# Performance work log

Measured on AMD Instinct MI355X. Metric: run time of the kernel, lower is better.

The kernel has to match this reference:

```python
import jax, jax.numpy as jnp
import numpy as np

EMBED_DIM = 512

def setup_inputs() -> dict:
    key = jax.random.key(0)
    ks = jax.random.split(key, 8)
    B, N, M, C = 4, 4096, 4096, EMBED_DIM
    s = 1.0 / np.sqrt(C)
    return {
        "rgb_features": jax.random.normal(ks[0], (B, N, C), jnp.float32),
        "depth_features": jax.random.normal(ks[1], (B, M, C), jnp.float32),
        "Wq": jax.random.normal(ks[2], (C, C), jnp.float32) * s,
        "bq": jnp.zeros((C,), jnp.float32),
        "Wk": jax.random.normal(ks[3], (C, C), jnp.float32) * s,
        "bk": jnp.zeros((C,), jnp.float32),
        "Wv": jax.random.normal(ks[4], (C, C), jnp.float32) * s,
        "bv": jnp.zeros((C,), jnp.float32),
    }

def reference(rgb_features, depth_features, Wq, bq, Wk, bk, Wv, bv):
    C = rgb_features.shape[-1]
    scale = C ** (-0.5)
    Q = rgb_features @ Wq + bq          # [B, N, C]
    K = depth_features @ Wk + bk        # [B, M, C]
    V = depth_features @ Wv + bv        # [B, M, C]
    scores = jnp.einsum('bnc,bmc->bnm', Q, K) * scale
    attn = jax.nn.softmax(scores, axis=-1)
    return jnp.einsum('bnm,bmc->bnc', attn, V)
```

## Files before the change

kernel.cpp:

```cpp
#include <hip/hip_runtime.h>
#include <hip/hip_bf16.h>
#include <stdint.h>


typedef unsigned short u16;
typedef __attribute__((ext_vector_type(8))) short bf16x8;
typedef __attribute__((ext_vector_type(16))) float f32x16;
typedef __attribute__((ext_vector_type(4))) unsigned short u16x4;

#define GLD_LDS16(g, l)                                                        \
  __builtin_amdgcn_global_load_lds(                                            \
      (const __attribute__((address_space(1))) unsigned int*)(g),              \
      (__attribute__((address_space(3))) unsigned int*)(l), 16, 0, 0)

__device__ __forceinline__ u16 f2bf(float f) {
  unsigned x = __float_as_uint(f);
  return (u16)((x + 0x7fffu + ((x >> 16) & 1u)) >> 16);
}
__device__ __forceinline__ float bf2f(short s) {
  return __uint_as_float((unsigned)(unsigned short)s << 16);
}

template <int TM, int TN, int BIAS_MODE, int OUT_MODE, int MINW>
__global__ __launch_bounds__(256, MINW) void gemm32(
    const u16* __restrict__ A, const u16* __restrict__ Bm,
    const float* __restrict__ bias, void* __restrict__ Cv, int M, int N, int K,
    long long sAb, long long sBb, long long sCb, float scale) {
  constexpr int WROWS = TM / 2;
  constexpr int WCOLS = TN / 2;
  constexpr int MSUB = WROWS / 32;
  constexpr int NSUB = WCOLS / 32;
  constexpr int CA = TM / 64;
  constexpr int CB = TN / 64;

  const int bz = blockIdx.z;
  A += (size_t)bz * sAb;
  Bm += (size_t)bz * sBb;

  const int bm = blockIdx.y * TM;
  const int bn = blockIdx.x * TN;

  __shared__ u16 As[2][TM * 32];
  __shared__ u16 Bs[2][TN * 32];

  const int tid = threadIdx.x;
  const int wave = tid >> 6;
  const int lane = tid & 63;
  const int ln31 = lane & 31;
  const int half = lane >> 5;
  const int wr = wave >> 1;
  const int wc = wave & 1;

  const int rowA = lane >> 2;
  const int swz = ((lane & 3) ^ ((rowA + (rowA >> 2)) & 3)) * 8;
  const int gl = (ln31 + (ln31 >> 2)) & 3;

  f32x16 acc[MSUB][NSUB] = {};

  auto stage = [&](int buf, int k0) {
#pragma unroll
    for (int r = 0; r < CA; ++r) {
      const int ch = wave * CA + r;
      GLD_LDS16(A + (size_t)(bm + ch * 16 + rowA) * K + k0 + swz,
                As[buf] + ch * 16 * 32);
    }
#pragma unroll
    for (int r = 0; r < CB; ++r) {
      const int ch = wave * CB + r;
      GLD_LDS16(Bm + (size_t)(bn + ch * 16 + rowA) * K + k0 + swz,
                Bs[buf] + ch * 16 * 32);
    }
  };

  const int niter = K >> 5;
  stage(0, 0);
  for (int it = 0; it < niter; ++it) {
    __syncthreads();
    if (it + 1 < niter) stage((it + 1) & 1, (it + 1) * 32);
    const int buf = it & 1;
#pragma unroll
    for (int kc = 0; kc < 2; ++kc) {
      const int p = ((kc * 2 + half) ^ gl) * 8;
      bf16x8 af[MSUB], bfv[NSUB];
#pragma unroll
      for (int mt = 0; mt < MSUB; ++mt)
        af[mt] =
            *(const bf16x8*)&As[buf][(wr * WROWS + mt * 32 + ln31) * 32 + p];
#pragma unroll
      for (int nt = 0; nt < NSUB; ++nt)
        bfv[nt] =
            *(const bf16x8*)&Bs[buf][(wc * WCOLS + nt * 32 + ln31) * 32 + p];
#pragma unroll
      for (int mt = 0; mt < MSUB; ++mt)
#pragma unroll
        for (int nt = 0; nt < NSUB; ++nt)
          acc[mt][nt] = __builtin_amdgcn_mfma_f32_32x32x16_bf16(
              af[mt], bfv[nt], acc[mt][nt], 0, 0, 0);
    }
  }

  const int crow0 = bm + wr * WROWS + 4 * half;
  const int ccol0 = bn + wc * WCOLS + ln31;
#pragma unroll
  for (int mt = 0; mt < MSUB; ++mt) {
#pragma unroll
    for (int nt = 0; nt < NSUB; ++nt) {
      const int col = ccol0 + nt * 32;
#pragma unroll
      for (int r = 0; r < 16; ++r) {
        const int row = crow0 + mt * 32 + (r & 3) + 8 * (r >> 2);
        float v = acc[mt][nt][r];
        if constexpr (BIAS_MODE == 1) v += bias[col];
        if constexpr (BIAS_MODE == 2) v += bias[row];
        const size_t idx = (size_t)bz * (size_t)sCb + (size_t)row * N + col;
        if constexpr (OUT_MODE == 0)
          ((u16*)Cv)[idx] = f2bf(v);
        else if constexpr (OUT_MODE == 1)
          ((float*)Cv)[idx] = v;
        else
          ((u16*)Cv)[idx] = f2bf(__expf(v * scale));
      }
    }
  }
}

__global__ __launch_bounds__(256, 2) void pv_gemm(
    const u16* __restrict__ P, const u16* __restrict__ Vt,
    float* __restrict__ O) {
  const int bz = blockIdx.z;
  const u16* A = P + (size_t)bz * (4096ull * 4096ull);
  const u16* B = Vt + (size_t)bz * (512ull * 4096ull);
  float* Ob = O + (size_t)bz * (4096ull * 512ull);

  const int bm = blockIdx.y * 64;
  const int bn = blockIdx.x * 256;

  __shared__ u16 As[2][64 * 32];
  __shared__ u16 Bs[2][256 * 32];
  __shared__ float den_s[64];

  const int tid = threadIdx.x;
  const int wave = tid >> 6;
  const int lane = tid & 63;
  const int ln31 = lane & 31;
  const int half = lane >> 5;

  const int rowA = lane >> 2;
  const int swz = ((lane & 3) ^ ((rowA + (rowA >> 2)) & 3)) * 8;
  const int gl = (ln31 + (ln31 >> 2)) & 3;

  f32x16 acc[2][2] = {};
  float rsum[2] = {0.f, 0.f};

  auto stage = [&](int buf, int k0) {
    GLD_LDS16(A + (size_t)(bm + wave * 16 + rowA) * 4096 + k0 + swz,
              As[buf] + wave * 16 * 32);
#pragma unroll
    for (int r = 0; r < 4; ++r) {
      const int ch = wave * 4 + r;
      GLD_LDS16(B + (size_t)(bn + ch * 16 + rowA) * 4096 + k0 + swz,
                Bs[buf] + ch * 16 * 32);
    }
  };

  stage(0, 0);
  for (int it = 0; it < 128; ++it) {
    __syncthreads();
    if (it + 1 < 128) stage((it + 1) & 1, (it + 1) * 32);
    const int buf = it & 1;
#pragma unroll
    for (int kc = 0; kc < 2; ++kc) {
      const int p = ((kc * 2 + half) ^ gl) * 8;
      bf16x8 af[2], bfv[2];
#pragma unroll
      for (int mt = 0; mt < 2; ++mt)
        af[mt] = *(const bf16x8*)&As[buf][(mt * 32 + ln31) * 32 + p];
#pragma unroll
      for (int nt = 0; nt < 2; ++nt)
        bfv[nt] =
            *(const bf16x8*)&Bs[buf][(wave * 64 + nt * 32 + ln31) * 32 + p];
#pragma unroll
      for (int mt = 0; mt < 2; ++mt) {
#pragma unroll
        for (int j = 0; j < 8; ++j) rsum[mt] += bf2f(af[mt][j]);
#pragma unroll
        for (int nt = 0; nt < 2; ++nt)
          acc[mt][nt] = __builtin_amdgcn_mfma_f32_32x32x16_bf16(
              af[mt], bfv[nt], acc[mt][nt], 0, 0, 0);
      }
    }
  }

#pragma unroll
  for (int mt = 0; mt < 2; ++mt) rsum[mt] += __shfl_xor(rsum[mt], 32, 64);
  __syncthreads();
  if (wave == 0 && half == 0) {
    den_s[ln31] = rsum[0];
    den_s[32 + ln31] = rsum[1];
  }
  __syncthreads();

  const int crow0 = 4 * half;
  const int ccol0 = bn + wave * 64 + ln31;
#pragma unroll
  for (int mt = 0; mt < 2; ++mt) {
#pragma unroll
    for (int r = 0; r < 16; ++r) {
      const int rl = crow0 + mt * 32 + (r & 3) + 8 * (r >> 2);
      const float rd = 1.0f / den_s[rl];
#pragma unroll
      for (int nt = 0; nt < 2; ++nt)
        Ob[(size_t)(bm + rl) * 512 + ccol0 + nt * 32] = acc[mt][nt][r] * rd;
    }
  }
}

__global__ __launch_bounds__(256) void cvt_pair(const float* __restrict__ x,
                                                const float* __restrict__ y,
                                                u16* __restrict__ ox,
                                                u16* __restrict__ oy, int n4) {
  const int i = blockIdx.x * 256 + threadIdx.x;
  if (i >= n4) return;
  const float4 a = ((const float4*)x)[i];
  const float4 b = ((const float4*)y)[i];
  u16x4 oa, ob;
  oa[0] = f2bf(a.x); oa[1] = f2bf(a.y); oa[2] = f2bf(a.z); oa[3] = f2bf(a.w);
  ob[0] = f2bf(b.x); ob[1] = f2bf(b.y); ob[2] = f2bf(b.z); ob[3] = f2bf(b.w);
  ((u16x4*)ox)[i] = oa;
  ((u16x4*)oy)[i] = ob;
}

__global__ __launch_bounds__(256) void wtrans_k(const float* __restrict__ W,
                                                u16* __restrict__ WT) {
  const int tr = blockIdx.y * 64;
  const int tc = blockIdx.x * 64;
  __shared__ float T[64][65];
  const int t = threadIdx.x;
  const int r0 = t >> 4;
  const int c0 = (t & 15) * 4;
#pragma unroll
  for (int rr = 0; rr < 4; ++rr) {
    const int row = rr * 16 + r0;
    const float4 w = *(const float4*)&W[(size_t)(tr + row) * 512 + tc + c0];
    T[row][c0 + 0] = w.x; T[row][c0 + 1] = w.y;
    T[row][c0 + 2] = w.z; T[row][c0 + 3] = w.w;
  }
  __syncthreads();
#pragma unroll
  for (int rr = 0; rr < 4; ++rr) {
    const int orow = rr * 16 + r0;
    u16x4 o;
#pragma unroll
    for (int j = 0; j < 4; ++j) o[j] = f2bf(T[c0 + j][orow]);
    *(u16x4*)&WT[(size_t)(tc + orow) * 512 + tr + c0] = o;
  }
}

extern "C" void kernel_launch(void* const* d_in, const int* in_sizes, int n_in,
                              void* d_out, int out_size, void* d_ws,
                              size_t ws_size, hipStream_t stream) {
  const float* rgb = (const float*)d_in[0];
  const float* dep = (const float*)d_in[1];
  const float* Wq = (const float*)d_in[2];
  const float* bq = (const float*)d_in[3];
  const float* Wk = (const float*)d_in[4];
  const float* bk = (const float*)d_in[5];
  const float* Wv = (const float*)d_in[6];
  const float* bv = (const float*)d_in[7];
  float* out = (float*)d_out;

  const int B = 4, N = 4096, M = 4096, C = 512;
  const size_t nBNC = (size_t)B * N * C;
  const float scale = 0.044194173824159216f;

  char* ws = (char*)d_ws;
  size_t off = 0;
  auto carve = [&](size_t bytes) -> void* {
    void* p = ws + off;
    off += (bytes + 255) & ~(size_t)255;
    return p;
  };
  u16* rgb_bf = (u16*)carve(nBNC * 2);
  u16* dep_bf = (u16*)carve(nBNC * 2);
  u16* WqT = (u16*)carve((size_t)C * C * 2);
  u16* WkT = (u16*)carve((size_t)C * C * 2);
  u16* WvT = (u16*)carve((size_t)C * C * 2);
  u16* Qb = (u16*)carve(nBNC * 2);
  u16* Kb = (u16*)carve(nBNC * 2);
  u16* Vt = (u16*)carve(nBNC * 2);
  u16* Sb = (u16*)carve((size_t)B * N * M * 2);

  const long long strQ = (long long)N * C;
  const long long strS = (long long)N * M;
  const long long strV = (long long)C * M;

  cvt_pair<<<8192, 256, 0, stream>>>(rgb, dep, rgb_bf, dep_bf, (int)(nBNC / 4));
  wtrans_k<<<dim3(8, 8), 256, 0, stream>>>(Wq, WqT);
  wtrans_k<<<dim3(8, 8), 256, 0, stream>>>(Wk, WkT);
  wtrans_k<<<dim3(8, 8), 256, 0, stream>>>(Wv, WvT);

  gemm32<128, 128, 1, 0, 4><<<dim3(4, 128, 1), 256, 0, stream>>>(
      rgb_bf, WqT, bq, Qb, 16384, 512, 512, 0, 0, 0, 1.f);
  gemm32<128, 128, 1, 0, 4><<<dim3(4, 128, 1), 256, 0, stream>>>(
      dep_bf, WkT, bk, Kb, 16384, 512, 512, 0, 0, 0, 1.f);
  gemm32<128, 128, 2, 0, 4><<<dim3(32, 4, 4), 256, 0, stream>>>(
      WvT, dep_bf, bv, Vt, 512, 4096, 512, 0, strQ, strV, 1.f);

  gemm32<128, 128, 0, 2, 4><<<dim3(32, 32, 4), 256, 0, stream>>>(
      Qb, Kb, nullptr, Sb, 4096, 4096, 512, strQ, strQ, strS, scale);

  pv_gemm<<<dim3(2, 64, 4), 256, 0, stream>>>(Sb, Vt, out);
}
```

Before: 383.5 us.

## Replace LDS-staged GEMM tiles with direct global-to-register double-buffered loads

All GEMM kernels stop staging A/B tiles through shared memory with async global-to-LDS loads and barriers. Each wave now loads its MFMA operand fragments directly from global memory into a two-deep register buffer, alternating compute and prefetch. This removes LDS traffic and per-iteration __syncthreads, but drops cross-wave reuse of tiles. Global/L2 traffic rises and access is strided per lane, and register pressure increases under a 3-block occupancy bound.

Result: slower. 718.6 us (+87.4%).

```diff
diff --git a/kernel.cpp b/kernel.cpp
--- a/kernel.cpp
+++ b/kernel.cpp
@@ -8,11 +8,6 @@
 typedef __attribute__((ext_vector_type(16))) float f32x16;
 typedef __attribute__((ext_vector_type(4))) unsigned short u16x4;
 
-#define GLD_LDS16(g, l)                                                        \
-  __builtin_amdgcn_global_load_lds(                                            \
-      (const __attribute__((address_space(1))) unsigned int*)(g),              \
-      (__attribute__((address_space(3))) unsigned int*)(l), 16, 0, 0)
-
 __device__ __forceinline__ u16 f2bf(float f) {
   unsigned x = __float_as_uint(f);
   return (u16)((x + 0x7fffu + ((x >> 16) & 1u)) >> 16);
@@ -21,90 +16,78 @@
   return __uint_as_float((unsigned)(unsigned short)s << 16);
 }
 
-template <int TM, int TN, int BIAS_MODE, int OUT_MODE, int MINW>
-__global__ __launch_bounds__(256, MINW) void gemm32(
+template <int BIAS_MODE, int OUT_MODE>
+__global__ __launch_bounds__(256, 3) void rd_gemm(
     const u16* __restrict__ A, const u16* __restrict__ Bm,
     const float* __restrict__ bias, void* __restrict__ Cv, int M, int N, int K,
     long long sAb, long long sBb, long long sCb, float scale) {
-  constexpr int WROWS = TM / 2;
-  constexpr int WCOLS = TN / 2;
-  constexpr int MSUB = WROWS / 32;
-  constexpr int NSUB = WCOLS / 32;
-  constexpr int CA = TM / 64;
-  constexpr int CB = TN / 64;
-
   const int bz = blockIdx.z;
   A += (size_t)bz * sAb;
   Bm += (size_t)bz * sBb;
-
-  const int bm = blockIdx.y * TM;
-  const int bn = blockIdx.x * TN;
-
-  __shared__ u16 As[2][TM * 32];
-  __shared__ u16 Bs[2][TN * 32];
-
+  const int bm = blockIdx.y * 128;
+  const int bn = blockIdx.x * 128;
   const int tid = threadIdx.x;
-  const int wave = tid >> 6;
-  const int lane = tid & 63;
-  const int ln31 = lane & 31;
-  const int half = lane >> 5;
-  const int wr = wave >> 1;
-  const int wc = wave & 1;
-
-  const int rowA = lane >> 2;
-  const int swz = ((lane & 3) ^ ((rowA + (rowA >> 2)) & 3)) * 8;
-  const int gl = (ln31 + (ln31 >> 2)) & 3;
-
-  f32x16 acc[MSUB][NSUB] = {};
-
-  auto stage = [&](int buf, int k0) {
-#pragma unroll
-    for (int r = 0; r < CA; ++r) {
-      const int ch = wave * CA + r;
-      GLD_LDS16(A + (size_t)(bm + ch * 16 + rowA) * K + k0 + swz,
-                As[buf] + ch * 16 * 32);
-    }
-#pragma unroll
-    for (int r = 0; r < CB; ++r) {
-      const int ch = wave * CB + r;
-      GLD_LDS16(Bm + (size_t)(bn + ch * 16 + rowA) * K + k0 + swz,
-                Bs[buf] + ch * 16 * 32);
-    }
+  const int wave = tid >> 6, lane = tid & 63;
+  const int ln31 = lane & 31, half = lane >> 5;
+  const int wr = wave >> 1, wc = wave & 1;
+
+  const u16* ap[2];
+  const u16* bp[2];
+#pragma unroll
+  for (int mt = 0; mt < 2; ++mt)
+    ap[mt] = A + (size_t)(bm + wr * 64 + mt * 32 + ln31) * K + half * 8;
+#pragma unroll
+  for (int nt = 0; nt < 2; ++nt)
+    bp[nt] = Bm + (size_t)(bn + wc * 64 + nt * 32 + ln31) * K + half * 8;
+
+  bf16x8 la[2][2][2], lb[2][2][2];
+  f32x16 acc[2][2] = {};
+
+  auto load = [&](int buf) {
+#pragma unroll
+    for (int mt = 0; mt < 2; ++mt) {
+#pragma unroll
+      for (int kc = 0; kc < 2; ++kc)
+        la[buf][mt][kc] = *(const bf16x8*)(ap[mt] + kc * 16);
+      ap[mt] += 32;
+    }
+#pragma unroll
+    for (int nt = 0; nt < 2; ++nt) {
+#pragma unroll
+      for (int kc = 0; kc < 2; ++kc)
+        lb[buf][nt][kc] = *(const bf16x8*)(bp[nt] + kc * 16);
+      bp[nt] += 32;
+    }
+  };
+  auto compute = [&](int buf) {
+#pragma unroll
+    for (int kc = 0; kc < 2; ++kc)
+#pragma unroll
+      for (int mt = 0; mt < 2; ++mt)
+#pragma unroll
+        for (int nt = 0; nt < 2; ++nt)
+          acc[mt][nt] = __builtin_amdgcn_mfma_f32_32x32x16_bf16(
+              la[buf][mt][kc], lb[buf][nt][kc], acc[mt][nt], 0, 0, 0);
   };
 
   const int niter = K >> 5;
-  stage(0, 0);
-  for (int it = 0; it < niter; ++it) {
-    __syncthreads();
-    if (it + 1 < niter) stage((it + 1) & 1, (it + 1) * 32);
-    const int buf = it & 1;
-#pragma unroll
-    for (int kc = 0; kc < 2; ++kc) {
-      const int p = ((kc * 2 + half) ^ gl) * 8;
-      bf16x8 af[MSUB], bfv[NSUB];
-#pragma unroll
-      for (int mt = 0; mt < MSUB; ++mt)
-        af[mt] =
-            *(const bf16x8*)&As[buf][(wr * WROWS + mt * 32 + ln31) * 32 + p];
-#pragma unroll
-      for (int nt = 0; nt < NSUB; ++nt)
-        bfv[nt] =
-            *(const bf16x8*)&Bs[buf][(wc * WCOLS + nt * 32 + ln31) * 32 + p];
-#pragma unroll
-      for (int mt = 0; mt < MSUB; ++mt)
-#pragma unroll
-        for (int nt = 0; nt < NSUB; ++nt)
-          acc[mt][nt] = __builtin_amdgcn_mfma_f32_32x32x16_bf16(
-              af[mt], bfv[nt], acc[mt][nt], 0, 0, 0);
-    }
-  }
-
-  const int crow0 = bm + wr * WROWS + 4 * half;
-  const int ccol0 = bn + wc * WCOLS + ln31;
-#pragma unroll
-  for (int mt = 0; mt < MSUB; ++mt) {
-#pragma unroll
-    for (int nt = 0; nt < NSUB; ++nt) {
+  load(0);
+  load(1);
+  for (int it = 0; it < niter - 2; it += 2) {
+    compute(0);
+    load(0);
+    compute(1);
+    load(1);
+  }
+  compute(0);
+  compute(1);
+
+  const int crow0 = bm + wr * 64 + 4 * half;
+  const int ccol0 = bn + wc * 64 + ln31;
+#pragma unroll
+  for (int mt = 0; mt < 2; ++mt) {
+#pragma unroll
+    for (int nt = 0; nt < 2; ++nt) {
       const int col = ccol0 + nt * 32;
 #pragma unroll
       for (int r = 0; r < 16; ++r) {
@@ -124,9 +107,9 @@
   }
 }
 
-__global__ __launch_bounds__(256, 2) void pv_gemm(
-    const u16* __restrict__ P, const u16* __restrict__ Vt,
-    float* __restrict__ O) {
+__global__ __launch_bounds__(256, 3) void rd_pv(const u16* __restrict__ P,
+                                                const u16* __restrict__ Vt,
+                                                float* __restrict__ O) {
   const int bz = blockIdx.z;
   const u16* A = P + (size_t)bz * (4096ull * 4096ull);
   const u16* B = Vt + (size_t)bz * (512ull * 4096ull);
@@ -135,65 +118,69 @@
   const int bm = blockIdx.y * 64;
   const int bn = blockIdx.x * 256;
 
-  __shared__ u16 As[2][64 * 32];
-  __shared__ u16 Bs[2][256 * 32];
   __shared__ float den_s[64];
 
   const int tid = threadIdx.x;
-  const int wave = tid >> 6;
-  const int lane = tid & 63;
-  const int ln31 = lane & 31;
-  const int half = lane >> 5;
-
-  const int rowA = lane >> 2;
-  const int swz = ((lane & 3) ^ ((rowA + (rowA >> 2)) & 3)) * 8;
-  const int gl = (ln31 + (ln31 >> 2)) & 3;
-
+  const int wave = tid >> 6, lane = tid & 63;
+  const int ln31 = lane & 31, half = lane >> 5;
+
+  const u16* ap[2];
+  const u16* bp[2];
+#pragma unroll
+  for (int mt = 0; mt < 2; ++mt)
+    ap[mt] = A + (size_t)(bm + mt * 32 + ln31) * 4096 + half * 8;
+#pragma unroll
+  for (int nt = 0; nt < 2; ++nt)
+    bp[nt] = B + (size_t)(bn + wave * 64 + nt * 32 + ln31) * 4096 + half * 8;
+
+  bf16x8 la[2][2][2], lb[2][2][2];
   f32x16 acc[2][2] = {};
   float rsum[2] = {0.f, 0.f};
 
-  auto stage = [&](int buf, int k0) {
-    GLD_LDS16(A + (size_t)(bm + wave * 16 + rowA) * 4096 + k0 + swz,
-              As[buf] + wave * 16 * 32);
-#pragma unroll
-    for (int r = 0; r < 4; ++r) {
-      const int ch = wave * 4 + r;
-      GLD_LDS16(B + (size_t)(bn + ch * 16 + rowA) * 4096 + k0 + swz,
-                Bs[buf] + ch * 16 * 32);
-    }
-  };
-
-  stage(0, 0);
-  for (int it = 0; it < 128; ++it) {
-    __syncthreads();
-    if (it + 1 < 128) stage((it + 1) & 1, (it + 1) * 32);
-    const int buf = it & 1;
+  auto load = [&](int buf) {
+#pragma unroll
+    for (int mt = 0; mt < 2; ++mt) {
+#pragma unroll
+      for (int kc = 0; kc < 2; ++kc)
+        la[buf][mt][kc] = *(const bf16x8*)(ap[mt] + kc * 16);
+      ap[mt] += 32;
+    }
+#pragma unroll
+    for (int nt = 0; nt < 2; ++nt) {
+#pragma unroll
+      for (int kc = 0; kc < 2; ++kc)
+        lb[buf][nt][kc] = *(const bf16x8*)(bp[nt] + kc * 16);
+      bp[nt] += 32;
+    }
+  };
+  auto compute = [&](int buf) {
 #pragma unroll
     for (int kc = 0; kc < 2; ++kc) {
-      const int p = ((kc * 2 + half) ^ gl) * 8;
-      bf16x8 af[2], bfv[2];
-#pragma unroll
-      for (int mt = 0; mt < 2; ++mt)
-        af[mt] = *(const bf16x8*)&As[buf][(mt * 32 + ln31) * 32 + p];
-#pragma unroll
-      for (int nt = 0; nt < 2; ++nt)
-        bfv[nt] =
-            *(const bf16x8*)&Bs[buf][(wave * 64 + nt * 32 + ln31) * 32 + p];
 #pragma unroll
       for (int mt = 0; mt < 2; ++mt) {
 #pragma unroll
-        for (int j = 0; j < 8; ++j) rsum[mt] += bf2f(af[mt][j]);
+        for (int j = 0; j < 8; ++j) rsum[mt] += bf2f(la[buf][mt][kc][j]);
 #pragma unroll
         for (int nt = 0; nt < 2; ++nt)
           acc[mt][nt] = __builtin_amdgcn_mfma_f32_32x32x16_bf16(
-              af[mt], bfv[nt], acc[mt][nt], 0, 0, 0);
+              la[buf][mt][kc], lb[buf][nt][kc], acc[mt][nt], 0, 0, 0);
       }
     }
-  }
+  };
+
+  load(0);
+  load(1);
+  for (int it = 0; it < 126; it += 2) {
+    compute(0);
+    load(0);
+    compute(1);
+    load(1);
+  }
+  compute(0);
+  compute(1);
 
 #pragma unroll
   for (int mt = 0; mt < 2; ++mt) rsum[mt] += __shfl_xor(rsum[mt], 32, 64);
-  __syncthreads();
   if (wave == 0 && half == 0) {
     den_s[ln31] = rsum[0];
     den_s[32 + ln31] = rsum[1];
@@ -299,15 +286,15 @@
   wtrans_k<<<dim3(8, 8), 256, 0, stream>>>(Wk, WkT);
   wtrans_k<<<dim3(8, 8), 256, 0, stream>>>(Wv, WvT);
 
-  gemm32<128, 128, 1, 0, 4><<<dim3(4, 128, 1), 256, 0, stream>>>(
+  rd_gemm<1, 0><<<dim3(4, 128, 1), 256, 0, stream>>>(
       rgb_bf, WqT, bq, Qb, 16384, 512, 512, 0, 0, 0, 1.f);
-  gemm32<128, 128, 1, 0, 4><<<dim3(4, 128, 1), 256, 0, stream>>>(
+  rd_gemm<1, 0><<<dim3(4, 128, 1), 256, 0, stream>>>(
       dep_bf, WkT, bk, Kb, 16384, 512, 512, 0, 0, 0, 1.f);
-  gemm32<128, 128, 2, 0, 4><<<dim3(32, 4, 4), 256, 0, stream>>>(
+  rd_gemm<2, 0><<<dim3(32, 4, 4), 256, 0, stream>>>(
       WvT, dep_bf, bv, Vt, 512, 4096, 512, 0, strQ, strV, 1.f);
 
-  gemm32<128, 128, 0, 2, 4><<<dim3(32, 32, 4), 256, 0, stream>>>(
+  rd_gemm<0, 2><<<dim3(32, 32, 4), 256, 0, stream>>>(
       Qb, Kb, nullptr, Sb, 4096, 4096, 512, strQ, strQ, strS, scale);
 
-  pv_gemm<<<dim3(2, 64, 4), 256, 0, stream>>>(Sb, Vt, out);
-}
+  rd_pv<<<dim3(2, 64, 4), 256, 0, stream>>>(Sb, Vt, out);
+}
```

## Register-prefetch GEMM pipeline with fused fp32-to-bf16 input conversion

Applied to the files above, without the earlier changes.

Replaces the global_load_lds direct-to-LDS staging with a register-staged pipeline that prefetches two k-steps ahead and writes to LDS after issuing the ds_reads. The fp32 inputs are converted to bf16 inside the projection GEMMs, which removes the separate conversion kernel and its bf16 round trip through memory. All GEMMs, including the PV step with row-sum normalisation, are unified under one templated kernel with explicit occupancy hints. This costs more VGPRs for the prefetch buffers, and global memory traffic now goes through registers.

After: 394.5 us. 1.03x slower.

```diff
diff --git a/kernel.cpp b/kernel.cpp
--- a/kernel.cpp
+++ b/kernel.cpp
@@ -8,107 +8,193 @@
 typedef __attribute__((ext_vector_type(16))) float f32x16;
 typedef __attribute__((ext_vector_type(4))) unsigned short u16x4;
 
-#define GLD_LDS16(g, l)                                                        \
-  __builtin_amdgcn_global_load_lds(                                            \
-      (const __attribute__((address_space(1))) unsigned int*)(g),              \
-      (__attribute__((address_space(3))) unsigned int*)(l), 16, 0, 0)
-
 __device__ __forceinline__ u16 f2bf(float f) {
   unsigned x = __float_as_uint(f);
   return (u16)((x + 0x7fffu + ((x >> 16) & 1u)) >> 16);
 }
+__device__ __forceinline__ unsigned pack2(float a, float b) {
+  return (unsigned)f2bf(a) | ((unsigned)f2bf(b) << 16);
+}
 __device__ __forceinline__ float bf2f(short s) {
   return __uint_as_float((unsigned)(unsigned short)s << 16);
 }
 
-template <int TM, int TN, int BIAS_MODE, int OUT_MODE, int MINW>
-__global__ __launch_bounds__(256, MINW) void gemm32(
-    const u16* __restrict__ A, const u16* __restrict__ Bm,
+template <int TM, int TN, int WC, bool AF32, bool BF32, int BIAS_MODE,
+          int OUT_MODE, int MINW>
+__global__ __launch_bounds__(256, MINW) void pgemm(
+    const void* __restrict__ Av, const void* __restrict__ Bv,
     const float* __restrict__ bias, void* __restrict__ Cv, int M, int N, int K,
     long long sAb, long long sBb, long long sCb, float scale) {
-  constexpr int WROWS = TM / 2;
-  constexpr int WCOLS = TN / 2;
-  constexpr int MSUB = WROWS / 32;
-  constexpr int NSUB = WCOLS / 32;
+  constexpr int WR = 4 / WC;
+  constexpr int WROWS = TM / WR;
+  constexpr int WCOLS = TN / WC;
   constexpr int CA = TM / 64;
   constexpr int CB = TN / 64;
 
   const int bz = blockIdx.z;
-  A += (size_t)bz * sAb;
-  Bm += (size_t)bz * sBb;
-
   const int bm = blockIdx.y * TM;
   const int bn = blockIdx.x * TN;
+  const int tid = threadIdx.x;
+  const int wave = tid >> 6, lane = tid & 63;
+  const int ln31 = lane & 31, half = lane >> 5;
+  const int wr = wave / WC;
+  const int wc = wave % WC;
+  const int gl = (ln31 + (ln31 >> 2)) & 3;
+
+  const float* Af = (const float*)Av + (size_t)bz * sAb;
+  const u16* Ab = (const u16*)Av + (size_t)bz * sAb;
+  const float* Bf = (const float*)Bv + (size_t)bz * sBb;
+  const u16* Bb = (const u16*)Bv + (size_t)bz * sBb;
 
   __shared__ u16 As[2][TM * 32];
   __shared__ u16 Bs[2][TN * 32];
-
-  const int tid = threadIdx.x;
-  const int wave = tid >> 6;
-  const int lane = tid & 63;
-  const int ln31 = lane & 31;
-  const int half = lane >> 5;
-  const int wr = wave >> 1;
-  const int wc = wave & 1;
-
-  const int rowA = lane >> 2;
-  const int swz = ((lane & 3) ^ ((rowA + (rowA >> 2)) & 3)) * 8;
-  const int gl = (ln31 + (ln31 >> 2)) & 3;
-
-  f32x16 acc[MSUB][NSUB] = {};
-
-  auto stage = [&](int buf, int k0) {
-#pragma unroll
-    for (int r = 0; r < CA; ++r) {
-      const int ch = wave * CA + r;
-      GLD_LDS16(A + (size_t)(bm + ch * 16 + rowA) * K + k0 + swz,
-                As[buf] + ch * 16 * 32);
-    }
-#pragma unroll
-    for (int r = 0; r < CB; ++r) {
-      const int ch = wave * CB + r;
-      GLD_LDS16(Bm + (size_t)(bn + ch * 16 + rowA) * K + k0 + swz,
-                Bs[buf] + ch * 16 * 32);
-    }
-  };
-
+  __shared__ float den_s[64];
+
+  int rA[CA], cA[CA], gA[CA];
+#pragma unroll
+  for (int i = 0; i < CA; ++i) {
+    const int c = tid + i * 256;
+    rA[i] = c >> 2;
+    cA[i] = c & 3;
+    gA[i] = (c & 3) ^ ((rA[i] + (rA[i] >> 2)) & 3);
+  }
+  int rB[CB], cB[CB], gB[CB];
+#pragma unroll
+  for (int i = 0; i < CB; ++i) {
+    const int c = tid + i * 256;
+    rB[i] = c >> 2;
+    cB[i] = c & 3;
+    gB[i] = (c & 3) ^ ((rB[i] + (rB[i] >> 2)) & 3);
+  }
+
+  float4 gaf[2][AF32 ? 2 * CA : 1];
+  uint4 gau[2][AF32 ? 1 : CA];
+  float4 gbf[2][BF32 ? 2 * CB : 1];
+  uint4 gbu[2][BF32 ? 1 : CB];
+
+  auto loadA = [&](int s, int k0) {
+#pragma unroll
+    for (int i = 0; i < CA; ++i) {
+      if constexpr (AF32) {
+        const float* p = Af + (size_t)(bm + rA[i]) * K + k0 + gA[i] * 8;
+        gaf[s][2 * i] = *(const float4*)p;
+        gaf[s][2 * i + 1] = *(const float4*)(p + 4);
+      } else {
+        gau[s][i] =
+            *(const uint4*)(Ab + (size_t)(bm + rA[i]) * K + k0 + gA[i] * 8);
+      }
+    }
+  };
+  auto loadB = [&](int s, int k0) {
+#pragma unroll
+    for (int i = 0; i < CB; ++i) {
+      if constexpr (BF32) {
+        const float* p = Bf + (size_t)(bn + rB[i]) * K + k0 + gB[i] * 8;
+        gbf[s][2 * i] = *(const float4*)p;
+        gbf[s][2 * i + 1] = *(const float4*)(p + 4);
+      } else {
+        gbu[s][i] =
+            *(const uint4*)(Bb + (size_t)(bn + rB[i]) * K + k0 + gB[i] * 8);
+      }
+    }
+  };
+  auto writeA = [&](int buf, int s) {
+#pragma unroll
+    for (int i = 0; i < CA; ++i) {
+      uint4 w;
+      if constexpr (AF32) {
+        const float4 x = gaf[s][2 * i], y = gaf[s][2 * i + 1];
+        w.x = pack2(x.x, x.y); w.y = pack2(x.z, x.w);
+        w.z = pack2(y.x, y.y); w.w = pack2(y.z, y.w);
+      } else {
+        w = gau[s][i];
+      }
+      *(uint4*)&As[buf][rA[i] * 32 + cA[i] * 8] = w;
+    }
+  };
+  auto writeB = [&](int buf, int s) {
+#pragma unroll
+    for (int i = 0; i < CB; ++i) {
+      uint4 w;
+      if constexpr (BF32) {
+        const float4 x = gbf[s][2 * i], y = gbf[s][2 * i + 1];
+        w.x = pack2(x.x, x.y); w.y = pack2(x.z, x.w);
+        w.z = pack2(y.x, y.y); w.w = pack2(y.z, y.w);
+      } else {
+        w = gbu[s][i];
+      }
+      *(uint4*)&Bs[buf][rB[i] * 32 + cB[i] * 8] = w;
+    }
+  };
+
+  f32x16 acc[2][2] = {};
+  float rsum[2] = {0.f, 0.f};
   const int niter = K >> 5;
-  stage(0, 0);
-  for (int it = 0; it < niter; ++it) {
+
+  loadA(0, 0); loadB(0, 0);
+  loadA(1, 32); loadB(1, 32);
+  writeA(0, 0); writeB(0, 0);
+  __syncthreads();
+
+#define KSTEP(IT, BUF)                                                         \
+  {                                                                            \
+    bf16x8 af[2][2], bfv[2][2];                                                \
+    _Pragma("unroll") for (int kc = 0; kc < 2; ++kc) {                         \
+      const int p = ((kc * 2 + half) ^ gl) * 8;                                \
+      _Pragma("unroll") for (int mt = 0; mt < 2; ++mt) af[kc][mt] =            \
+          *(const bf16x8*)&As[BUF][(wr * WROWS + mt * 32 + ln31) * 32 + p];    \
+      _Pragma("unroll") for (int nt = 0; nt < 2; ++nt) bfv[kc][nt] =           \
+          *(const bf16x8*)&Bs[BUF][(wc * WCOLS + nt * 32 + ln31) * 32 + p];    \
+    }                                                                          \
+    if ((IT) + 2 < niter) {                                                    \
+      loadA(BUF, ((IT) + 2) * 32);                                             \
+      loadB(BUF, ((IT) + 2) * 32);                                             \
+    }                                                                          \
+    if ((IT) + 1 < niter) {                                                    \
+      writeA(BUF ^ 1, BUF ^ 1);                                                \
+      writeB(BUF ^ 1, BUF ^ 1);                                                \
+    }                                                                          \
+    _Pragma("unroll") for (int kc = 0; kc < 2; ++kc) {                         \
+      _Pragma("unroll") for (int mt = 0; mt < 2; ++mt) {                       \
+        if constexpr (OUT_MODE == 3) {                                         \
+          _Pragma("unroll") for (int j = 0; j < 8; ++j) rsum[mt] +=            \
+              bf2f(af[kc][mt][j]);                                             \
+        }                                                                      \
+        _Pragma("unroll") for (int nt = 0; nt < 2; ++nt) acc[mt][nt] =         \
+            __builtin_amdgcn_mfma_f32_32x32x16_bf16(af[kc][mt], bfv[kc][nt],   \
+                                                    acc[mt][nt], 0, 0, 0);     \
+      }                                                                        \
+    }                                                                          \
+    __syncthreads();                                                           \
+  }
+
+  for (int it = 0; it < niter; it += 2) {
+    KSTEP(it, 0);
+    KSTEP(it + 1, 1);
+  }
+#undef KSTEP
+
+  if constexpr (OUT_MODE == 3) {
+#pragma unroll
+    for (int mt = 0; mt < 2; ++mt) rsum[mt] += __shfl_xor(rsum[mt], 32, 64);
+    if (wave == 0 && half == 0) {
+      den_s[ln31] = rsum[0];
+      den_s[32 + ln31] = rsum[1];
+    }
     __syncthreads();
-    if (it + 1 < niter) stage((it + 1) & 1, (it + 1) * 32);
-    const int buf = it & 1;
-#pragma unroll
-    for (int kc = 0; kc < 2; ++kc) {
-      const int p = ((kc * 2 + half) ^ gl) * 8;
-      bf16x8 af[MSUB], bfv[NSUB];
-#pragma unroll
-      for (int mt = 0; mt < MSUB; ++mt)
-        af[mt] =
-            *(const bf16x8*)&As[buf][(wr * WROWS + mt * 32 + ln31) * 32 + p];
-#pragma unroll
-      for (int nt = 0; nt < NSUB; ++nt)
-        bfv[nt] =
-            *(const bf16x8*)&Bs[buf][(wc * WCOLS + nt * 32 + ln31) * 32 + p];
-#pragma unroll
-      for (int mt = 0; mt < MSUB; ++mt)
-#pragma unroll
-        for (int nt = 0; nt < NSUB; ++nt)
-          acc[mt][nt] = __builtin_amdgcn_mfma_f32_32x32x16_bf16(
-              af[mt], bfv[nt], acc[mt][nt], 0, 0, 0);
-    }
   }
 
   const int crow0 = bm + wr * WROWS + 4 * half;
   const int ccol0 = bn + wc * WCOLS + ln31;
 #pragma unroll
-  for (int mt = 0; mt < MSUB; ++mt) {
-#pragma unroll
-    for (int nt = 0; nt < NSUB; ++nt) {
+  for (int mt = 0; mt < 2; ++mt) {
+#pragma unroll
+    for (int nt = 0; nt < 2; ++nt) {
       const int col = ccol0 + nt * 32;
 #pragma unroll
       for (int r = 0; r < 16; ++r) {
-        const int row = crow0 + mt * 32 + (r & 3) + 8 * (r >> 2);
+        const int rl = wr * WROWS + 4 * half + mt * 32 + (r & 3) + 8 * (r >> 2);
+        const int row = bm + rl;
         float v = acc[mt][nt][r];
         if constexpr (BIAS_MODE == 1) v += bias[col];
         if constexpr (BIAS_MODE == 2) v += bias[row];
@@ -117,117 +203,13 @@
           ((u16*)Cv)[idx] = f2bf(v);
         else if constexpr (OUT_MODE == 1)
           ((float*)Cv)[idx] = v;
+        else if constexpr (OUT_MODE == 2)
+          ((u16*)Cv)[idx] = f2bf(__expf(v * scale));
         else
-          ((u16*)Cv)[idx] = f2bf(__expf(v * scale));
-      }
-    }
-  }
-}
-
-__global__ __launch_bounds__(256, 2) void pv_gemm(
-    const u16* __restrict__ P, const u16* __restrict__ Vt,
-    float* __restrict__ O) {
-  const int bz = blockIdx.z;
-  const u16* A = P + (size_t)bz * (4096ull * 4096ull);
-  const u16* B = Vt + (size_t)bz * (512ull * 4096ull);
-  float* Ob = O + (size_t)bz * (4096ull * 512ull);
-
-  const int bm = blockIdx.y * 64;
-  const int bn = blockIdx.x * 256;
-
-  __shared__ u16 As[2][64 * 32];
-  __shared__ u16 Bs[2][256 * 32];
-  __shared__ float den_s[64];
-
-  const int tid = threadIdx.x;
-  const int wave = tid >> 6;
-  const int lane = tid & 63;
-  const int ln31 = lane & 31;
-  const int half = lane >> 5;
-
-  const int rowA = lane >> 2;
-  const int swz = ((lane & 3) ^ ((rowA + (rowA >> 2)) & 3)) * 8;
-  const int gl = (ln31 + (ln31 >> 2)) & 3;
-
-  f32x16 acc[2][2] = {};
-  float rsum[2] = {0.f, 0.f};
-
-  auto stage = [&](int buf, int k0) {
-    GLD_LDS16(A + (size_t)(bm + wave * 16 + rowA) * 4096 + k0 + swz,
-              As[buf] + wave * 16 * 32);
-#pragma unroll
-    for (int r = 0; r < 4; ++r) {
-      const int ch = wave * 4 + r;
-      GLD_LDS16(B + (size_t)(bn + ch * 16 + rowA) * 4096 + k0 + swz,
-                Bs[buf] + ch * 16 * 32);
-    }
-  };
-
-  stage(0, 0);
-  for (int it = 0; it < 128; ++it) {
-    __syncthreads();
-    if (it + 1 < 128) stage((it + 1) & 1, (it + 1) * 32);
-    const int buf = it & 1;
-#pragma unroll
-    for (int kc = 0; kc < 2; ++kc) {
-      const int p = ((kc * 2 + half) ^ gl) * 8;
-      bf16x8 af[2], bfv[2];
-#pragma unroll
-      for (int mt = 0; mt < 2; ++mt)
-        af[mt] = *(const bf16x8*)&As[buf][(mt * 32 + ln31) * 32 + p];
-#pragma unroll
-      for (int nt = 0; nt < 2; ++nt)
-        bfv[nt] =
-            *(const bf16x8*)&Bs[buf][(wave * 64 + nt * 32 + ln31) * 32 + p];
-#pragma unroll
-      for (int mt = 0; mt < 2; ++mt) {
-#pragma unroll
-        for (int j = 0; j < 8; ++j) rsum[mt] += bf2f(af[mt][j]);
-#pragma unroll
-        for (int nt = 0; nt < 2; ++nt)
-          acc[mt][nt] = __builtin_amdgcn_mfma_f32_32x32x16_bf16(
-              af[mt], bfv[nt], acc[mt][nt], 0, 0, 0);
-      }
-    }
-  }
-
-#pragma unroll
-  for (int mt = 0; mt < 2; ++mt) rsum[mt] += __shfl_xor(rsum[mt], 32, 64);
-  __syncthreads();
-  if (wave == 0 && half == 0) {
-    den_s[ln31] = rsum[0];
-    den_s[32 + ln31] = rsum[1];
-  }
-  __syncthreads();
-
-  const int crow0 = 4 * half;
-  const int ccol0 = bn + wave * 64 + ln31;
-#pragma unroll
-  for (int mt = 0; mt < 2; ++mt) {
-#pragma unroll
-    for (int r = 0; r < 16; ++r) {
-      const int rl = crow0 + mt * 32 + (r & 3) + 8 * (r >> 2);
-      const float rd = 1.0f / den_s[rl];
-#pragma unroll
-      for (int nt = 0; nt < 2; ++nt)
-        Ob[(size_t)(bm + rl) * 512 + ccol0 + nt * 32] = acc[mt][nt][r] * rd;
-    }
-  }
-}
-
-__global__ __launch_bounds__(256) void cvt_pair(const float* __restrict__ x,
-                                                const float* __restrict__ y,
-                                                u16* __restrict__ ox,
-                                                u16* __restrict__ oy, int n4) {
-  const int i = blockIdx.x * 256 + threadIdx.x;
-  if (i >= n4) return;
-  const float4 a = ((const float4*)x)[i];
-  const float4 b = ((const float4*)y)[i];
-  u16x4 oa, ob;
-  oa[0] = f2bf(a.x); oa[1] = f2bf(a.y); oa[2] = f2bf(a.z); oa[3] = f2bf(a.w);
-  ob[0] = f2bf(b.x); ob[1] = f2bf(b.y); ob[2] = f2bf(b.z); ob[3] = f2bf(b.w);
-  ((u16x4*)ox)[i] = oa;
-  ((u16x4*)oy)[i] = ob;
+          ((float*)Cv)[idx] = v * (1.0f / den_s[rl]);
+      }
+    }
+  }
 }
 
 __global__ __launch_bounds__(256) void wtrans_k(const float* __restrict__ W,
@@ -280,8 +262,6 @@
     off += (bytes + 255) & ~(size_t)255;
     return p;
   };
-  u16* rgb_bf = (u16*)carve(nBNC * 2);
-  u16* dep_bf = (u16*)carve(nBNC * 2);
   u16* WqT = (u16*)carve((size_t)C * C * 2);
   u16* WkT = (u16*)carve((size_t)C * C * 2);
   u16* WvT = (u16*)carve((size_t)C * C * 2);
@@ -294,20 +274,21 @@
   const long long strS = (long long)N * M;
   const long long strV = (long long)C * M;
 
-  cvt_pair<<<8192, 256, 0, stream>>>(rgb, dep, rgb_bf, dep_bf, (int)(nBNC / 4));
   wtrans_k<<<dim3(8, 8), 256, 0, stream>>>(Wq, WqT);
   wtrans_k<<<dim3(8, 8), 256, 0, stream>>>(Wk, WkT);
   wtrans_k<<<dim3(8, 8), 256, 0, stream>>>(Wv, WvT);
 
-  gemm32<128, 128, 1, 0, 4><<<dim3(4, 128, 1), 256, 0, stream>>>(
-      rgb_bf, WqT, bq, Qb, 16384, 512, 512, 0, 0, 0, 1.f);
-  gemm32<128, 128, 1, 0, 4><<<dim3(4, 128, 1), 256, 0, stream>>>(
-      dep_bf, WkT, bk, Kb, 16384, 512, 512, 0, 0, 0, 1.f);
-  gemm32<128, 128, 2, 0, 4><<<dim3(32, 4, 4), 256, 0, stream>>>(
-      WvT, dep_bf, bv, Vt, 512, 4096, 512, 0, strQ, strV, 1.f);
-
-  gemm32<128, 128, 0, 2, 4><<<dim3(32, 32, 4), 256, 0, stream>>>(
-      Qb, Kb, nullptr, Sb, 4096, 4096, 512, strQ, strQ, strS, scale);
-
-  pv_gemm<<<dim3(2, 64, 4), 256, 0, stream>>>(Sb, Vt, out);
-}
+  pgemm<128, 128, 2, true, false, 1, 0, 2><<<dim3(4, 128, 1), 256, 0, stream>>>(
+      rgb, WqT, bq, Qb, 16384, 512, 512, 0, 0, 0, 1.f);
+  pgemm<128, 128, 2, true, false, 1, 0, 2><<<dim3(4, 128, 1), 256, 0, stream>>>(
+      dep, WkT, bk, Kb, 16384, 512, 512, 0, 0, 0, 1.f);
+  pgemm<128, 128, 2, false, true, 2, 0, 2><<<dim3(32, 4, 4), 256, 0, stream>>>(
+      WvT, dep, bv, Vt, 512, 4096, 512, 0, strQ, strV, 1.f);
+
+  pgemm<128, 128, 2, false, false, 0, 2, 3>
+      <<<dim3(32, 32, 4), 256, 0, stream>>>(Qb, Kb, nullptr, Sb, 4096, 4096,
+                                            512, strQ, strQ, strS, scale);
+
+  pgemm<64, 256, 4, false, false, 0, 3, 2><<<dim3(2, 64, 4), 256, 0, stream>>>(
+      Sb, Vt, nullptr, out, 4096, 512, 4096, strS, strV, strQ, 1.f);
+}
```
